# Performance work log

Hardware: AMD Instinct MI355X
Metric: run time of the kernel (lower is better)

The kernel has to match this reference:

```python
import jax, jax.numpy as jnp
import numpy as np

N_NODES = 100000
N_EDGES = 1600000
D = 128  # in_features


def setup_inputs() -> dict:
    key = jax.random.key(0)
    k1, k2, k3 = jax.random.split(key, 3)
    node_embeddings = jax.random.normal(k1, (N_NODES, D), dtype=jnp.float32)
    edge_index = jax.random.randint(k2, (2, N_EDGES), 0, N_NODES, dtype=jnp.int64)
    # attn_fc: Linear(2*D, 2) -> weight [2, 2*D], bias [2]
    W = jax.random.normal(k3, (2, 2 * D), dtype=jnp.float32) * (1.0 / np.sqrt(2 * D))
    b = jnp.zeros((2,), dtype=jnp.float32)
    return {"node_embeddings": node_embeddings, "edge_index": edge_index, "W": W, "b": b}


def reference(node_embeddings, edge_index, W, b):
    # Gather endpoint embeddings per edge, concat -> [E, 2*D]
    row, col = edge_index[0], edge_index[1]
    edge_feature = jnp.concatenate(
        [node_embeddings[row], node_embeddings[col]], axis=-1
    )  # [E, 2D]
    attn_scores = edge_feature @ W.T + b  # [E, 2]
    attn_scores = jax.nn.softmax(attn_scores, axis=-1)
    # dropout is identity in eval mode
    return attn_scores
```

## Files before the change

kernel.cpp:

```cpp
#include <hip/hip_runtime.h>

static constexpr int kNodes = 100000;
static constexpr int kEdges = 1600000;
static constexpr int kD     = 128;

typedef float fx4 __attribute__((ext_vector_type(4)));

__global__ __launch_bounds__(256) void node_pre(const float* __restrict__ emb,
                                                const float* __restrict__ W,
                                                float* __restrict__ h) {
    const int l  = threadIdx.x & 15;
    const int c0 = l * 8;

    fx4 w0a = *(const fx4*)&W[c0],       w0b = *(const fx4*)&W[c0 + 4];
    fx4 w1a = *(const fx4*)&W[256 + c0], w1b = *(const fx4*)&W[256 + c0 + 4];
    fx4 w2a = *(const fx4*)&W[128 + c0], w2b = *(const fx4*)&W[128 + c0 + 4];
    fx4 w3a = *(const fx4*)&W[384 + c0], w3b = *(const fx4*)&W[384 + c0 + 4];

    const int group   = (blockIdx.x * blockDim.x + threadIdx.x) >> 4;
    const int ngroups = (gridDim.x * blockDim.x) >> 4;

    for (int n = group; n < kNodes; n += ngroups) {
        const fx4* row = (const fx4*)(emb + (size_t)n * kD + c0);
        fx4 ea = row[0];
        fx4 eb = row[1];

        float p0 = ea.x*w0a.x + ea.y*w0a.y + ea.z*w0a.z + ea.w*w0a.w
                 + eb.x*w0b.x + eb.y*w0b.y + eb.z*w0b.z + eb.w*w0b.w;
        float p1 = ea.x*w1a.x + ea.y*w1a.y + ea.z*w1a.z + ea.w*w1a.w
                 + eb.x*w1b.x + eb.y*w1b.y + eb.z*w1b.z + eb.w*w1b.w;
        float p2 = ea.x*w2a.x + ea.y*w2a.y + ea.z*w2a.z + ea.w*w2a.w
                 + eb.x*w2b.x + eb.y*w2b.y + eb.z*w2b.z + eb.w*w2b.w;
        float p3 = ea.x*w3a.x + ea.y*w3a.y + ea.z*w3a.z + ea.w*w3a.w
                 + eb.x*w3b.x + eb.y*w3b.y + eb.z*w3b.z + eb.w*w3b.w;

        float sendU = (l & 1) ? p0 : p1;
        float keepU = (l & 1) ? p1 : p0;
        float u = keepU + __shfl_xor(sendU, 1);
        float sendW = (l & 1) ? p2 : p3;
        float keepW = (l & 1) ? p3 : p2;
        float w = keepW + __shfl_xor(sendW, 1);
        float sendX = (l & 2) ? u : w;
        float keepX = (l & 2) ? w : u;
        float x = keepX + __shfl_xor(sendX, 2);
        x += __shfl_xor(x, 4);
        x += __shfl_xor(x, 8);

        if (l < 4) h[n * 4 + l] = x;
    }
}

__global__ __launch_bounds__(256) void edge_attn(const void* __restrict__ eiv,
                                                 const float* __restrict__ h,
                                                 const float* __restrict__ b,
                                                 float* __restrict__ out) {
    const unsigned long long* ei64 = (const unsigned long long*)eiv;
    unsigned long long hi = ei64[threadIdx.x & 63] >> 32;
    const bool is64 = (__ballot(hi != 0ull) == 0ull);

    const int e4 = blockIdx.x * blockDim.x + threadIdx.x;
    if (e4 >= kEdges / 4) return;

    int r[4], c[4];
    if (is64) {
        const unsigned long long* rr = ei64 + 4 * e4;
        const unsigned long long* cc = ei64 + kEdges + 4 * e4;
#pragma unroll
        for (int k = 0; k < 4; ++k) {
            r[k] = (int)rr[k];
            c[k] = (int)cc[k];
        }
    } else {
        const int* ei32 = (const int*)eiv;
#pragma unroll
        for (int k = 0; k < 4; ++k) {
            r[k] = ei32[4 * e4 + k];
            c[k] = ei32[kEdges + 4 * e4 + k];
        }
    }

    const fx4* h4 = (const fx4*)h;
    const float b0 = b[0], b1 = b[1];

    float res[8];
#pragma unroll
    for (int k = 0; k < 4; ++k) {
        fx4 hr = h4[r[k]];
        fx4 hc = h4[c[k]];
        float s0 = hr.x + hc.z + b0;
        float s1 = hr.y + hc.w + b1;
        float m  = fmaxf(s0, s1);
        float x0 = __expf(s0 - m);
        float x1 = __expf(s1 - m);
        float inv = 1.0f / (x0 + x1);
        res[2*k]     = x0 * inv;
        res[2*k + 1] = x1 * inv;
    }

    fx4* o4 = (fx4*)out;
    fx4 oa = {res[0], res[1], res[2], res[3]};
    fx4 ob = {res[4], res[5], res[6], res[7]};
    o4[2 * e4]     = oa;
    o4[2 * e4 + 1] = ob;
}

extern "C" void kernel_launch(void* const* d_in, const int* in_sizes, int n_in,
                              void* d_out, int out_size, void* d_ws, size_t ws_size,
                              hipStream_t stream) {
    const float* emb = (const float*)d_in[0];
    const void*  ei  = d_in[1];
    const float* W   = (const float*)d_in[2];
    const float* b   = (const float*)d_in[3];
    float* out = (float*)d_out;

    float* h = (float*)d_ws;

    node_pre<<<(kNodes * 16 / 4 + 255) / 256, 256, 0, stream>>>(emb, W, h);

    edge_attn<<<(kEdges / 4 + 255) / 256, 256, 0, stream>>>(ei, h, b, out);
}
```

Measured before the change: 33.36 us.

## Precompute logit differences per node and use sigmoid form in edge kernel

```diff
diff --git a/kernel.cpp b/kernel.cpp
--- a/kernel.cpp
+++ b/kernel.cpp
@@ -8,100 +8,72 @@
 
 __global__ __launch_bounds__(256) void node_pre(const float* __restrict__ emb,
                                                 const float* __restrict__ W,
-                                                float* __restrict__ h) {
+                                                float* __restrict__ uv) {
     const int l  = threadIdx.x & 15;
     const int c0 = l * 8;
 
     fx4 w0a = *(const fx4*)&W[c0],       w0b = *(const fx4*)&W[c0 + 4];
     fx4 w1a = *(const fx4*)&W[256 + c0], w1b = *(const fx4*)&W[256 + c0 + 4];
+    fx4 dua = w1a - w0a, dub = w1b - w0b;
     fx4 w2a = *(const fx4*)&W[128 + c0], w2b = *(const fx4*)&W[128 + c0 + 4];
     fx4 w3a = *(const fx4*)&W[384 + c0], w3b = *(const fx4*)&W[384 + c0 + 4];
+    fx4 dva = w3a - w2a, dvb = w3b - w2b;
 
-    const int group   = (blockIdx.x * blockDim.x + threadIdx.x) >> 4;
-    const int ngroups = (gridDim.x * blockDim.x) >> 4;
+    const int n = (blockIdx.x * blockDim.x + threadIdx.x) >> 4;
+    if (n >= kNodes) return;
 
-    for (int n = group; n < kNodes; n += ngroups) {
-        const fx4* row = (const fx4*)(emb + (size_t)n * kD + c0);
-        fx4 ea = row[0];
-        fx4 eb = row[1];
+    const fx4* row = (const fx4*)(emb + (size_t)n * kD + c0);
+    fx4 ea = row[0];
+    fx4 eb = row[1];
 
-        float p0 = ea.x*w0a.x + ea.y*w0a.y + ea.z*w0a.z + ea.w*w0a.w
-                 + eb.x*w0b.x + eb.y*w0b.y + eb.z*w0b.z + eb.w*w0b.w;
-        float p1 = ea.x*w1a.x + ea.y*w1a.y + ea.z*w1a.z + ea.w*w1a.w
-                 + eb.x*w1b.x + eb.y*w1b.y + eb.z*w1b.z + eb.w*w1b.w;
-        float p2 = ea.x*w2a.x + ea.y*w2a.y + ea.z*w2a.z + ea.w*w2a.w
-                 + eb.x*w2b.x + eb.y*w2b.y + eb.z*w2b.z + eb.w*w2b.w;
-        float p3 = ea.x*w3a.x + ea.y*w3a.y + ea.z*w3a.z + ea.w*w3a.w
-                 + eb.x*w3b.x + eb.y*w3b.y + eb.z*w3b.z + eb.w*w3b.w;
+    float pu = ea.x*dua.x + ea.y*dua.y + ea.z*dua.z + ea.w*dua.w
+             + eb.x*dub.x + eb.y*dub.y + eb.z*dub.z + eb.w*dub.w;
+    float pv = ea.x*dva.x + ea.y*dva.y + ea.z*dva.z + ea.w*dva.w
+             + eb.x*dvb.x + eb.y*dvb.y + eb.z*dvb.z + eb.w*dvb.w;
 
-        float sendU = (l & 1) ? p0 : p1;
-        float keepU = (l & 1) ? p1 : p0;
-        float u = keepU + __shfl_xor(sendU, 1);
-        float sendW = (l & 1) ? p2 : p3;
-        float keepW = (l & 1) ? p3 : p2;
-        float w = keepW + __shfl_xor(sendW, 1);
-        float sendX = (l & 2) ? u : w;
-        float keepX = (l & 2) ? w : u;
-        float x = keepX + __shfl_xor(sendX, 2);
-        x += __shfl_xor(x, 4);
-        x += __shfl_xor(x, 8);
+    float keep = (l & 1) ? pv : pu;
+    float send = (l & 1) ? pu : pv;
+    float x = keep + __shfl_xor(send, 1);
+    x += __shfl_xor(x, 2);
+    x += __shfl_xor(x, 4);
+    x += __shfl_xor(x, 8);
 
-        if (l < 4) h[n * 4 + l] = x;
-    }
+    if (l < 2) uv[n * 2 + l] = x;
 }
 
 __global__ __launch_bounds__(256) void edge_attn(const void* __restrict__ eiv,
-                                                 const float* __restrict__ h,
+                                                 const float* __restrict__ uv,
                                                  const float* __restrict__ b,
                                                  float* __restrict__ out) {
     const unsigned long long* ei64 = (const unsigned long long*)eiv;
     unsigned long long hi = ei64[threadIdx.x & 63] >> 32;
     const bool is64 = (__ballot(hi != 0ull) == 0ull);
 
-    const int e4 = blockIdx.x * blockDim.x + threadIdx.x;
-    if (e4 >= kEdges / 4) return;
+    const int e2 = blockIdx.x * blockDim.x + threadIdx.x;
+    if (e2 >= kEdges / 2) return;
 
-    int r[4], c[4];
+    int r0, r1, c0i, c1i;
     if (is64) {
-        const unsigned long long* rr = ei64 + 4 * e4;
-        const unsigned long long* cc = ei64 + kEdges + 4 * e4;
-#pragma unroll
-        for (int k = 0; k < 4; ++k) {
-            r[k] = (int)rr[k];
-            c[k] = (int)cc[k];
-        }
+        const unsigned long long* rr = ei64 + 2 * e2;
+        const unsigned long long* cc = ei64 + kEdges + 2 * e2;
+        r0  = (int)rr[0]; r1  = (int)rr[1];
+        c0i = (int)cc[0]; c1i = (int)cc[1];
     } else {
         const int* ei32 = (const int*)eiv;
-#pragma unroll
-        for (int k = 0; k < 4; ++k) {
-            r[k] = ei32[4 * e4 + k];
-            c[k] = ei32[kEdges + 4 * e4 + k];
-        }
+        r0  = ei32[2 * e2];          r1  = ei32[2 * e2 + 1];
+        c0i = ei32[kEdges + 2 * e2]; c1i = ei32[kEdges + 2 * e2 + 1];
     }
 
-    const fx4* h4 = (const fx4*)h;
-    const float b0 = b[0], b1 = b[1];
+    const float db = b[1] - b[0];
 
-    float res[8];
-#pragma unroll
-    for (int k = 0; k < 4; ++k) {
-        fx4 hr = h4[r[k]];
-        fx4 hc = h4[c[k]];
-        float s0 = hr.x + hc.z + b0;
-        float s1 = hr.y + hc.w + b1;
-        float m  = fmaxf(s0, s1);
-        float x0 = __expf(s0 - m);
-        float x1 = __expf(s1 - m);
-        float inv = 1.0f / (x0 + x1);
-        res[2*k]     = x0 * inv;
-        res[2*k + 1] = x1 * inv;
-    }
+    float d0 = uv[2 * r0] + uv[2 * c0i + 1] + db;
+    float d1 = uv[2 * r1] + uv[2 * c1i + 1] + db;
 
-    fx4* o4 = (fx4*)out;
-    fx4 oa = {res[0], res[1], res[2], res[3]};
-    fx4 ob = {res[4], res[5], res[6], res[7]};
-    o4[2 * e4]     = oa;
-    o4[2 * e4 + 1] = ob;
+    float p00 = __builtin_amdgcn_rcpf(1.0f + __expf(d0));
+    float p10 = __builtin_amdgcn_rcpf(1.0f + __expf(d1));
+
+    fx4 o = {p00, 1.0f - p00, p10, 1.0f - p10};
+    ((fx4*)out)[e2] = o;
 }
 
 extern "C" void kernel_launch(void* const* d_in, const int* in_sizes, int n_in,
@@ -113,9 +85,9 @@
     const float* b   = (const float*)d_in[3];
     float* out = (float*)d_out;
 
-    float* h = (float*)d_ws;
+    float* uv = (float*)d_ws;
 
-    node_pre<<<(kNodes * 16 / 4 + 255) / 256, 256, 0, stream>>>(emb, W, h);
+    node_pre<<<(kNodes * 16 + 255) / 256, 256, 0, stream>>>(emb, W, uv);
 
-    edge_attn<<<(kEdges / 4 + 255) / 256, 256, 0, stream>>>(ei, h, b, out);
+    edge_attn<<<(kEdges / 2 + 255) / 256, 256, 0, stream>>>(ei, uv, b, out);
 }
```

Result: faster. 32.54 us (-2.5%).
